# Optimization experiments

Hardware: AMD Instinct MI355X
Metric: run time of the kernel (lower is better)

The kernel has to match this reference:

```python
import jax, jax.numpy as jnp
import numpy as np

SCALE = 0.08838834764831845  # 1/sqrt(head_dim=128)


def setup_inputs() -> dict:
    key = jax.random.key(0)
    ks = jax.random.split(key, 5)
    B, H, D = 16, 8, 128          # batch (decode seqs), kv heads, head_dim
    BS, BPS = 16, 128             # block_size, blocks per sequence
    NBLK = B * BPS                # total cache blocks (2048)
    CTX = 2048                    # context length per sequence
    q = jax.random.normal(ks[0], (B, H, D), jnp.float32)
    k = jax.random.normal(ks[1], (B, H, D), jnp.float32)
    v = jax.random.normal(ks[2], (B, H, D), jnp.float32)
    k_cache = jax.random.normal(ks[3], (NBLK, BS, H, D), jnp.float32)
    v_cache = jax.random.normal(ks[4], (NBLK, BS, H, D), jnp.float32)
    # each sequence owns a distinct contiguous set of blocks
    block_tables = jnp.arange(B * BPS, dtype=jnp.int32).reshape(B, BPS)
    context_lens = jnp.full((B,), CTX, dtype=jnp.int32)
    # slot for the newest token (position CTX-1) of each sequence
    last = CTX - 1
    slot_mapping = block_tables[:, last // BS] * BS + (last % BS)
    return {"q": q, "k": k, "v": v, "k_cache": k_cache, "v_cache": v_cache,
            "slot_mapping": slot_mapping.astype(jnp.int32),
            "block_tables": block_tables, "context_lens": context_lens}


def reference(q, k, v, k_cache, v_cache, slot_mapping, block_tables, context_lens):
    # ---- store_kvcache: scatter new k/v tokens into paged caches ----
    nblk, bs, H, D = k_cache.shape
    k_cache = k_cache.reshape(nblk * bs, H, D).at[slot_mapping].set(k).reshape(nblk, bs, H, D)
    v_cache = v_cache.reshape(nblk * bs, H, D).at[slot_mapping].set(v).reshape(nblk, bs, H, D)

    # ---- _sdpa_decode: paged gather + masked attention (q_per_seq = 1) ----
    B, nb = block_tables.shape
    T = nb * bs                              # max tokens per sequence
    token_idx = jnp.arange(T, dtype=jnp.int32)
    block_idx = token_idx // bs
    token_off = token_idx % bs
    block_ids = block_tables[:, block_idx]   # [B, T]
    k_all = k_cache[block_ids, token_off]    # [B, T, H, D]
    v_all = v_cache[block_ids, token_off]    # [B, T, H, D]

    valid = token_idx[None, :] < context_lens[:, None]           # [B, T]
    q_pos = context_lens - 1                                     # q_per_seq == 1
    causal = token_idx[None, :] <= q_pos[:, None]                # [B, T]
    mask = valid & causal

    scores = jnp.einsum("bhd,bthd->bht", q, k_all) * SCALE       # [B, H, T]
    scores = jnp.where(mask[:, None, :], scores, -jnp.inf)
    p = jax.nn.softmax(scores, axis=-1)
    out = jnp.einsum("bht,bthd->bhd", p, v_all)                  # [B, H, D]
    return out
```

## Files before the change

### kernel.cpp

```cpp
#include <hip/hip_runtime.h>
#include <math.h>

#define B_ 16
#define H_ 8
#define D_ 128
#define BS_ 16
#define BPS_ 128
#define T_ (BPS_ * BS_)
#define ROW_ (H_ * D_)
#define SCALE_ 0.08838834764831845f

typedef float f32x4 __attribute__((ext_vector_type(4)));

template<int NS>
__global__ __launch_bounds__(64, 4) void attn_partial(
    const float* __restrict__ q,
    const float* __restrict__ knew,
    const float* __restrict__ vnew,
    const float* __restrict__ kc,
    const float* __restrict__ vc,
    const int* __restrict__ btab,
    const int* __restrict__ clen,
    float2* __restrict__ ws_ml,
    float* __restrict__ ws_o)
{
    constexpr int CHUNK = T_ / NS;
    constexpr int NB = CHUNK / 4;
    static_assert(CHUNK % 4 == 0, "CHUNK multiple of 4");

    const int c = blockIdx.x;
    const int b = blockIdx.y;
    const int lane = threadIdx.x;
    const int h = lane >> 3;
    const int e = (lane & 7) * 4;
    const int ctx = clen[b];
    const int cs = c * CHUNK;

    f32x4 q4[4];
    #pragma unroll
    for (int i = 0; i < 4; ++i)
        q4[i] = *(const f32x4*)(q + (size_t)b * ROW_ + h * 128 + i * 32 + e);

    float sc[CHUNK];

    #pragma unroll
    for (int bt = 0; bt < NB; ++bt) {
        f32x4 kb[4][4];
        #pragma unroll
        for (int u = 0; u < 4; ++u) {
            const int tg = cs + bt * 4 + u;
            const int blk = btab[b * BPS_ + (tg >> 4)];
            const float* rb = (tg == ctx - 1)
                ? (knew + (size_t)b * ROW_)
                : (kc + ((size_t)blk * BS_ + (tg & 15)) * ROW_);
            #pragma unroll
            for (int i = 0; i < 4; ++i)
                kb[u][i] = __builtin_nontemporal_load(
                    (const f32x4*)(rb + h * 128 + i * 32 + e));
        }
        #pragma unroll
        for (int u = 0; u < 4; ++u) {
            const int tg = cs + bt * 4 + u;
            float s = 0.f;
            #pragma unroll
            for (int i = 0; i < 4; ++i)
                s += q4[i].x * kb[u][i].x + q4[i].y * kb[u][i].y
                   + q4[i].z * kb[u][i].z + q4[i].w * kb[u][i].w;
            s += __shfl_xor(s, 1);
            s += __shfl_xor(s, 2);
            s += __shfl_xor(s, 4);
            sc[bt * 4 + u] = (tg < ctx) ? s * SCALE_ : -INFINITY;
        }
    }

    float m = -INFINITY;
    #pragma unroll
    for (int t = 0; t < CHUNK; ++t) m = fmaxf(m, sc[t]);
    m = fmaxf(m, -1e30f);
    float l = 0.f;
    #pragma unroll
    for (int t = 0; t < CHUNK; ++t) {
        sc[t] = __expf(sc[t] - m);
        l += sc[t];
    }

    f32x4 acc[4];
    #pragma unroll
    for (int i = 0; i < 4; ++i) acc[i] = (f32x4)(0.f);

    #pragma unroll
    for (int bt = 0; bt < NB; ++bt) {
        f32x4 vb[4][4];
        #pragma unroll
        for (int u = 0; u < 4; ++u) {
            const int tg = cs + bt * 4 + u;
            const int blk = btab[b * BPS_ + (tg >> 4)];
            const float* rb = (tg == ctx - 1)
                ? (vnew + (size_t)b * ROW_)
                : (vc + ((size_t)blk * BS_ + (tg & 15)) * ROW_);
            #pragma unroll
            for (int i = 0; i < 4; ++i)
                vb[u][i] = __builtin_nontemporal_load(
                    (const f32x4*)(rb + h * 128 + i * 32 + e));
        }
        #pragma unroll
        for (int u = 0; u < 4; ++u) {
            const float pw = sc[bt * 4 + u];
            #pragma unroll
            for (int i = 0; i < 4; ++i)
                acc[i] += pw * vb[u][i];
        }
    }

    #pragma unroll
    for (int i = 0; i < 4; ++i)
        *(f32x4*)(ws_o + ((size_t)(b * H_ + h) * NS + c) * D_ + i * 32 + e) = acc[i];
    if ((lane & 7) == 0)
        ws_ml[(size_t)c * (B_ * H_) + b * H_ + h] = make_float2(m, l);
}

template<int NS>
__global__ __launch_bounds__(128) void attn_reduce(
    const float2* __restrict__ ws_ml,
    const float* __restrict__ ws_o,
    float* __restrict__ out)
{
    const int bh = blockIdx.x;
    const int tid = threadIdx.x;

    __shared__ float s_co[NS];
    __shared__ float s_lg;

    if (tid < 64) {
        float2 ml[NS / 64];
        float m = -INFINITY;
        #pragma unroll
        for (int r = 0; r < NS / 64; ++r) {
            ml[r] = ws_ml[(size_t)(r * 64 + tid) * (B_ * H_) + bh];
            m = fmaxf(m, ml[r].x);
        }
        m = fmaxf(m, __shfl_xor(m, 32));
        m = fmaxf(m, __shfl_xor(m, 16));
        m = fmaxf(m, __shfl_xor(m, 8));
        m = fmaxf(m, __shfl_xor(m, 4));
        m = fmaxf(m, __shfl_xor(m, 2));
        m = fmaxf(m, __shfl_xor(m, 1));
        float lw = 0.f;
        #pragma unroll
        for (int r = 0; r < NS / 64; ++r) {
            const float co = __expf(ml[r].x - m);
            s_co[r * 64 + tid] = co;
            lw += ml[r].y * co;
        }
        lw += __shfl_xor(lw, 32);
        lw += __shfl_xor(lw, 16);
        lw += __shfl_xor(lw, 8);
        lw += __shfl_xor(lw, 4);
        lw += __shfl_xor(lw, 2);
        lw += __shfl_xor(lw, 1);
        if (tid == 0) s_lg = lw;
    }
    __syncthreads();

    float acc = 0.f;
    #pragma unroll 8
    for (int cc = 0; cc < NS; ++cc)
        acc += s_co[cc] * ws_o[((size_t)bh * NS + cc) * D_ + tid];
    out[(size_t)bh * D_ + tid] = acc / s_lg;
}

template<int NS>
static void launch_all(const float* q, const float* knew, const float* vnew,
                       const float* kc, const float* vc,
                       const int* btab, const int* clen,
                       float* ws, float* out, hipStream_t stream)
{
    float2* ws_ml = (float2*)ws;
    float* ws_o = ws + 2 * B_ * H_ * NS;
    attn_partial<NS><<<dim3(NS, B_), 64, 0, stream>>>(q, knew, vnew, kc, vc,
                                                      btab, clen, ws_ml, ws_o);
    attn_reduce<NS><<<dim3(B_ * H_), 128, 0, stream>>>(ws_ml, ws_o, out);
}

extern "C" void kernel_launch(void* const* d_in, const int* in_sizes, int n_in,
                              void* d_out, int out_size, void* d_ws, size_t ws_size,
                              hipStream_t stream) {
    const float* q    = (const float*)d_in[0];
    const float* knew = (const float*)d_in[1];
    const float* vnew = (const float*)d_in[2];
    const float* kc   = (const float*)d_in[3];
    const float* vc   = (const float*)d_in[4];
    const int* btab = (const int*)d_in[6];
    const int* clen = (const int*)d_in[7];
    float* out = (float*)d_out;
    float* ws  = (float*)d_ws;

    const size_t need256 = (size_t)B_ * H_ * 256 * (2 + D_) * sizeof(float);
    const size_t need128 = (size_t)B_ * H_ * 128 * (2 + D_) * sizeof(float);
    if (ws_size >= need256)      launch_all<256>(q, knew, vnew, kc, vc, btab, clen, ws, out, stream);
    else if (ws_size >= need128) launch_all<128>(q, knew, vnew, kc, vc, btab, clen, ws, out, stream);
    else                         launch_all<64>(q, knew, vnew, kc, vc, btab, clen, ws, out, stream);
}
```

Before: 286.6 us.

## Prefetch K and V together in partial kernel and vectorize split reduce

For the two-batch chunk case (NS=256), the partial kernel now issues the first V batch's loads alongside both K batches, before the scores are computed. The second V batch is loaded while the first is being accumulated. This raises memory-level parallelism and lowers occupancy to 2 waves, trading registers for more loads in flight. The reduce kernel moves to 256 threads that each read float4s over a strided subset of splits, combines the partial sums through shared memory, and uses nontemporal loads and stores for the workspace.

```diff
diff --git a/kernel.cpp b/kernel.cpp
--- a/kernel.cpp
+++ b/kernel.cpp
@@ -13,7 +13,7 @@
 typedef float f32x4 __attribute__((ext_vector_type(4)));
 
 template<int NS>
-__global__ __launch_bounds__(64, 4) void attn_partial(
+__global__ __launch_bounds__(64, 2) void attn_partial(
     const float* __restrict__ q,
     const float* __restrict__ knew,
     const float* __restrict__ vnew,
@@ -36,91 +36,140 @@
     const int ctx = clen[b];
     const int cs = c * CHUNK;
 
+    auto krow = [&](int u) -> const float* {
+        const int tg = cs + u;
+        const int blk = btab[b * BPS_ + (tg >> 4)];
+        return (tg == ctx - 1) ? (knew + (size_t)b * ROW_)
+                               : (kc + ((size_t)blk * BS_ + (tg & 15)) * ROW_);
+    };
+    auto vrow = [&](int u) -> const float* {
+        const int tg = cs + u;
+        const int blk = btab[b * BPS_ + (tg >> 4)];
+        return (tg == ctx - 1) ? (vnew + (size_t)b * ROW_)
+                               : (vc + ((size_t)blk * BS_ + (tg & 15)) * ROW_);
+    };
+    auto ld4 = [&](f32x4 (&dst)[4], const float* rb) {
+        #pragma unroll
+        for (int i = 0; i < 4; ++i)
+            dst[i] = __builtin_nontemporal_load(
+                (const f32x4*)(rb + h * 128 + i * 32 + e));
+    };
+
     f32x4 q4[4];
     #pragma unroll
     for (int i = 0; i < 4; ++i)
         q4[i] = *(const f32x4*)(q + (size_t)b * ROW_ + h * 128 + i * 32 + e);
 
+    auto dot = [&](const f32x4 (&kb)[4]) -> float {
+        float s = 0.f;
+        #pragma unroll
+        for (int i = 0; i < 4; ++i)
+            s += q4[i].x * kb[i].x + q4[i].y * kb[i].y
+               + q4[i].z * kb[i].z + q4[i].w * kb[i].w;
+        s += __shfl_xor(s, 1);
+        s += __shfl_xor(s, 2);
+        s += __shfl_xor(s, 4);
+        return s;
+    };
+
     float sc[CHUNK];
+    f32x4 acc[4];
+    #pragma unroll
+    for (int i = 0; i < 4; ++i) acc[i] = (f32x4)(0.f);
+
+    if constexpr (NB == 2) {
+        f32x4 k0[4][4], k1[4][4], v0[4][4], v1[4][4];
+        #pragma unroll
+        for (int u = 0; u < 4; ++u) ld4(k0[u], krow(u));
+        #pragma unroll
+        for (int u = 0; u < 4; ++u) ld4(v0[u], vrow(u));
+        #pragma unroll
+        for (int u = 0; u < 4; ++u) ld4(k1[u], krow(4 + u));
+
+        #pragma unroll
+        for (int u = 0; u < 4; ++u) {
+            const float s = dot(k0[u]);
+            sc[u] = (cs + u < ctx) ? s * SCALE_ : -INFINITY;
+        }
+        #pragma unroll
+        for (int u = 0; u < 4; ++u) {
+            const float s = dot(k1[u]);
+            sc[4 + u] = (cs + 4 + u < ctx) ? s * SCALE_ : -INFINITY;
+        }
+
+        float m = -INFINITY;
+        #pragma unroll
+        for (int t = 0; t < 8; ++t) m = fmaxf(m, sc[t]);
+        m = fmaxf(m, -1e30f);
+        float l = 0.f;
+        #pragma unroll
+        for (int t = 0; t < 8; ++t) { sc[t] = __expf(sc[t] - m); l += sc[t]; }
+
+        #pragma unroll
+        for (int u = 0; u < 4; ++u) {
+            const float pw = sc[u];
+            #pragma unroll
+            for (int i = 0; i < 4; ++i) acc[i] += pw * v0[u][i];
+        }
+        #pragma unroll
+        for (int u = 0; u < 4; ++u) ld4(v1[u], vrow(4 + u));
+        #pragma unroll
+        for (int u = 0; u < 4; ++u) {
+            const float pw = sc[4 + u];
+            #pragma unroll
+            for (int i = 0; i < 4; ++i) acc[i] += pw * v1[u][i];
+        }
+
+        #pragma unroll
+        for (int i = 0; i < 4; ++i)
+            __builtin_nontemporal_store(acc[i],
+                (f32x4*)(ws_o + ((size_t)(b * H_ + h) * NS + c) * D_ + i * 32 + e));
+        if ((lane & 7) == 0)
+            ws_ml[(size_t)c * (B_ * H_) + b * H_ + h] = make_float2(m, l);
+        return;
+    }
 
     #pragma unroll
     for (int bt = 0; bt < NB; ++bt) {
         f32x4 kb[4][4];
         #pragma unroll
-        for (int u = 0; u < 4; ++u) {
-            const int tg = cs + bt * 4 + u;
-            const int blk = btab[b * BPS_ + (tg >> 4)];
-            const float* rb = (tg == ctx - 1)
-                ? (knew + (size_t)b * ROW_)
-                : (kc + ((size_t)blk * BS_ + (tg & 15)) * ROW_);
-            #pragma unroll
-            for (int i = 0; i < 4; ++i)
-                kb[u][i] = __builtin_nontemporal_load(
-                    (const f32x4*)(rb + h * 128 + i * 32 + e));
-        }
-        #pragma unroll
-        for (int u = 0; u < 4; ++u) {
-            const int tg = cs + bt * 4 + u;
-            float s = 0.f;
-            #pragma unroll
-            for (int i = 0; i < 4; ++i)
-                s += q4[i].x * kb[u][i].x + q4[i].y * kb[u][i].y
-                   + q4[i].z * kb[u][i].z + q4[i].w * kb[u][i].w;
-            s += __shfl_xor(s, 1);
-            s += __shfl_xor(s, 2);
-            s += __shfl_xor(s, 4);
-            sc[bt * 4 + u] = (tg < ctx) ? s * SCALE_ : -INFINITY;
-        }
-    }
-
+        for (int u = 0; u < 4; ++u) ld4(kb[u], krow(bt * 4 + u));
+        #pragma unroll
+        for (int u = 0; u < 4; ++u) {
+            const float s = dot(kb[u]);
+            sc[bt * 4 + u] = (cs + bt * 4 + u < ctx) ? s * SCALE_ : -INFINITY;
+        }
+    }
     float m = -INFINITY;
     #pragma unroll
     for (int t = 0; t < CHUNK; ++t) m = fmaxf(m, sc[t]);
     m = fmaxf(m, -1e30f);
     float l = 0.f;
     #pragma unroll
-    for (int t = 0; t < CHUNK; ++t) {
-        sc[t] = __expf(sc[t] - m);
-        l += sc[t];
-    }
-
-    f32x4 acc[4];
-    #pragma unroll
-    for (int i = 0; i < 4; ++i) acc[i] = (f32x4)(0.f);
+    for (int t = 0; t < CHUNK; ++t) { sc[t] = __expf(sc[t] - m); l += sc[t]; }
 
     #pragma unroll
     for (int bt = 0; bt < NB; ++bt) {
         f32x4 vb[4][4];
         #pragma unroll
-        for (int u = 0; u < 4; ++u) {
-            const int tg = cs + bt * 4 + u;
-            const int blk = btab[b * BPS_ + (tg >> 4)];
-            const float* rb = (tg == ctx - 1)
-                ? (vnew + (size_t)b * ROW_)
-                : (vc + ((size_t)blk * BS_ + (tg & 15)) * ROW_);
-            #pragma unroll
-            for (int i = 0; i < 4; ++i)
-                vb[u][i] = __builtin_nontemporal_load(
-                    (const f32x4*)(rb + h * 128 + i * 32 + e));
-        }
+        for (int u = 0; u < 4; ++u) ld4(vb[u], vrow(bt * 4 + u));
         #pragma unroll
         for (int u = 0; u < 4; ++u) {
             const float pw = sc[bt * 4 + u];
             #pragma unroll
-            for (int i = 0; i < 4; ++i)
-                acc[i] += pw * vb[u][i];
-        }
-    }
-
+            for (int i = 0; i < 4; ++i) acc[i] += pw * vb[u][i];
+        }
+    }
     #pragma unroll
     for (int i = 0; i < 4; ++i)
-        *(f32x4*)(ws_o + ((size_t)(b * H_ + h) * NS + c) * D_ + i * 32 + e) = acc[i];
+        __builtin_nontemporal_store(acc[i],
+            (f32x4*)(ws_o + ((size_t)(b * H_ + h) * NS + c) * D_ + i * 32 + e));
     if ((lane & 7) == 0)
         ws_ml[(size_t)c * (B_ * H_) + b * H_ + h] = make_float2(m, l);
 }
 
 template<int NS>
-__global__ __launch_bounds__(128) void attn_reduce(
+__global__ __launch_bounds__(256) void attn_reduce(
     const float2* __restrict__ ws_ml,
     const float* __restrict__ ws_o,
     float* __restrict__ out)
@@ -130,6 +179,7 @@
 
     __shared__ float s_co[NS];
     __shared__ float s_lg;
+    __shared__ f32x4 s_t[8][32];
 
     if (tid < 64) {
         float2 ml[NS / 64];
@@ -162,11 +212,23 @@
     }
     __syncthreads();
 
-    float acc = 0.f;
-    #pragma unroll 8
-    for (int cc = 0; cc < NS; ++cc)
-        acc += s_co[cc] * ws_o[((size_t)bh * NS + cc) * D_ + tid];
-    out[(size_t)bh * D_ + tid] = acc / s_lg;
+    const int ss = tid >> 5;
+    const int ln = tid & 31;
+    f32x4 a = (f32x4)(0.f);
+    #pragma unroll 4
+    for (int cc = ss; cc < NS; cc += 8)
+        a += s_co[cc] * __builtin_nontemporal_load(
+            (const f32x4*)(ws_o + ((size_t)bh * NS + cc) * D_ + ln * 4));
+    s_t[ss][ln] = a;
+    __syncthreads();
+
+    if (tid < 32) {
+        f32x4 r = (f32x4)(0.f);
+        #pragma unroll
+        for (int s = 0; s < 8; ++s) r += s_t[s][tid];
+        r *= (1.0f / s_lg);
+        *(f32x4*)(out + (size_t)bh * D_ + tid * 4) = r;
+    }
 }
 
 template<int NS>
@@ -179,7 +241,7 @@
     float* ws_o = ws + 2 * B_ * H_ * NS;
     attn_partial<NS><<<dim3(NS, B_), 64, 0, stream>>>(q, knew, vnew, kc, vc,
                                                       btab, clen, ws_ml, ws_o);
-    attn_reduce<NS><<<dim3(B_ * H_), 128, 0, stream>>>(ws_ml, ws_o, out);
+    attn_reduce<NS><<<dim3(B_ * H_), 256, 0, stream>>>(ws_ml, ws_o, out);
 }
 
 extern "C" void kernel_launch(void* const* d_in, const int* in_sizes, int n_in,
```

After: 273.7 us. -4.5%, faster.
